# Optimization experiments

Hardware: AMD Instinct MI355X
Metric: run time of the kernel (lower is better)

Reference implementation:

```python
import jax, jax.numpy as jnp
import numpy as np

B, S, D, H = 2, 2048, 768, 12
HD = D // H  # head_dim = 64


def setup_inputs() -> dict:
    key = jax.random.key(0)
    ks = jax.random.split(key, 9)
    s = 1.0 / np.sqrt(D)
    return {
        "x": jax.random.normal(ks[0], (B, S, D), dtype=jnp.float32),
        "Wq": jax.random.normal(ks[1], (D, D), dtype=jnp.float32) * s,
        "bq": jnp.zeros((D,), dtype=jnp.float32),
        "Wk": jax.random.normal(ks[2], (D, D), dtype=jnp.float32) * s,
        "bk": jnp.zeros((D,), dtype=jnp.float32),
        "Wv": jax.random.normal(ks[3], (D, D), dtype=jnp.float32) * s,
        "bv": jnp.zeros((D,), dtype=jnp.float32),
        "Wo": jax.random.normal(ks[4], (D, D), dtype=jnp.float32) * s,
        "bo": jnpp if False else jnp.zeros((D,), dtype=jnp.float32),
    }


def reference(x, Wq, bq, Wk, bk, Wv, bv, Wo, bo):
    b, s, d = x.shape
    # projections, split heads: [b, h, s, hd]
    def proj(W, bias):
        y = x @ W + bias
        return y.reshape(b, s, H, HD).transpose(0, 2, 1, 3)

    q = proj(Wq, bq)
    k = proj(Wk, bk)
    v = proj(Wv, bv)

    scale = 1.0 / jnp.sqrt(jnp.float32(HD))
    scores = jnp.einsum("bhqd,bhkd->bhqk", q, k) * scale
    causal = jnp.tril(jnp.ones((s, s), dtype=bool))  # True where allowed
    scores = jnp.where(causal, scores, -jnp.inf)
    attn = jax.nn.softmax(scores, axis=-1)
    ctx = jnp.einsum("bhqk,bhkd->bhqd", attn, v)
    ctx = ctx.transpose(0, 2, 1, 3).reshape(b, s, d)
    return ctx @ Wo + bo
```

## Files before the change

kernel.cpp:

```cpp
#include <hip/hip_runtime.h>
#include <stdint.h>

typedef unsigned short u16;
typedef __attribute__((ext_vector_type(8))) short s16x8;
typedef __attribute__((ext_vector_type(4))) float f32x4;
typedef __attribute__((ext_vector_type(16))) float f32x16;

#define MFMA_BF16(a, b, c) __builtin_amdgcn_mfma_f32_16x16x32_bf16((a), (b), (c), 0, 0, 0)
#define MFMA32(a, b, c) __builtin_amdgcn_mfma_f32_32x32x16_bf16((a), (b), (c), 0, 0, 0)

typedef const __attribute__((address_space(1))) uint32_t* gas1_t;
typedef __attribute__((address_space(3))) uint32_t* las3_t;
#define GLDS16(dst, src) __builtin_amdgcn_global_load_lds((gas1_t)(src), (las3_t)(dst), 16, 0, 0)

static __device__ __forceinline__ u16 f2bf(float f) {
    uint32_t u = __float_as_uint(f);
    u = (u + 0x7fffu + ((u >> 16) & 1u)) >> 16;
    return (u16)u;
}
static __device__ __forceinline__ uint32_t pk2bf(float a, float b) {
    return (uint32_t)f2bf(a) | ((uint32_t)f2bf(b) << 16);
}

__global__ void k_cvt_bf16(const float* __restrict__ in, u16* __restrict__ out) {
    int i = (blockIdx.x * 256 + threadIdx.x) * 8;
    f32x4 a = *(const f32x4*)(in + i);
    f32x4 b = *(const f32x4*)(in + i + 4);
    s16x8 r;
    r[0] = (short)f2bf(a[0]); r[1] = (short)f2bf(a[1]);
    r[2] = (short)f2bf(a[2]); r[3] = (short)f2bf(a[3]);
    r[4] = (short)f2bf(b[0]); r[5] = (short)f2bf(b[1]);
    r[6] = (short)f2bf(b[2]); r[7] = (short)f2bf(b[3]);
    *(s16x8*)(out + i) = r;
}

__global__ void k_transpose_w(const float* __restrict__ w0, const float* __restrict__ w1,
                              const float* __restrict__ w2, const float* __restrict__ w3,
                              u16* __restrict__ t0, u16* __restrict__ t1,
                              u16* __restrict__ t2, u16* __restrict__ t3) {
    __shared__ float tile[32][33];
    const float* W; u16* T;
    switch (blockIdx.z) {
        case 0:  W = w0; T = t0; break;
        case 1:  W = w1; T = t1; break;
        case 2:  W = w2; T = t2; break;
        default: W = w3; T = t3; break;
    }
    int n0 = blockIdx.x * 32, k0 = blockIdx.y * 32;
    int tx = threadIdx.x, ty = threadIdx.y;
#pragma unroll
    for (int i = 0; i < 4; ++i)
        tile[ty + 8 * i][tx] = W[(size_t)(k0 + ty + 8 * i) * 768 + n0 + tx];
    __syncthreads();
#pragma unroll
    for (int i = 0; i < 4; ++i)
        T[(size_t)(n0 + ty + 8 * i) * 768 + k0 + tx] = f2bf(tile[tx][ty + 8 * i]);
}

__global__ __launch_bounds__(256) void k_gemm_qkv(
        const u16* __restrict__ A,
        const u16* __restrict__ btq, const u16* __restrict__ btk, const u16* __restrict__ btv,
        const float* __restrict__ bq, const float* __restrict__ bk, const float* __restrict__ bv,
        u16* __restrict__ outq, u16* __restrict__ outk, u16* __restrict__ outv) {
    __shared__ u16 lA[128 * 64];
    __shared__ u16 lB[64 * 64];
    const int bx = blockIdx.x, sel = bx / 12, nb = bx - sel * 12;
    const u16* Bt; const float* bias;
    if (sel == 0)      { Bt = btq; bias = bq; }
    else if (sel == 1) { Bt = btk; bias = bk; }
    else               { Bt = btv; bias = bv; }
    const int t = threadIdx.x, lane = t & 63, w = t >> 6;
    const int wr = w >> 1, wc = w & 1;
    const int c = lane & 15, g = lane >> 4;
    const int m0 = blockIdx.y * 128, n0 = nb * 64;
    f32x4 acc[4][2] = {};
    const int lr = lane >> 3, lg = lane & 7;
    const int swz8 = 8 * (lg ^ lr);
    const u16* gA = A  + (size_t)(m0 + w * 8 + lr) * 768 + swz8;
    const u16* gB = Bt + (size_t)(n0 + w * 8 + lr) * 768 + swz8;
    for (int kb = 0; kb < 768; kb += 64) {
#pragma unroll
        for (int j = 0; j < 4; ++j)
            GLDS16(&lA[j * 2048 + w * 512], gA + (size_t)j * 32 * 768 + kb);
#pragma unroll
        for (int j = 0; j < 2; ++j)
            GLDS16(&lB[j * 2048 + w * 512], gB + (size_t)j * 32 * 768 + kb);
        __syncthreads();
#pragma unroll
        for (int kh = 0; kh < 2; ++kh) {
            s16x8 af[4], bfr[2];
            const int gg = kh * 4 + g;
#pragma unroll
            for (int i = 0; i < 4; ++i) {
                const int ra = wr * 64 + i * 16 + c;
                af[i] = *(const s16x8*)&lA[ra * 64 + 8 * (gg ^ (ra & 7))];
            }
#pragma unroll
            for (int j = 0; j < 2; ++j) {
                const int rb = wc * 32 + j * 16 + c;
                bfr[j] = *(const s16x8*)&lB[rb * 64 + 8 * (gg ^ (rb & 7))];
            }
#pragma unroll
            for (int i = 0; i < 4; ++i)
#pragma unroll
                for (int j = 0; j < 2; ++j)
                    acc[i][j] = MFMA_BF16(af[i], bfr[j], acc[i][j]);
        }
        __syncthreads();
    }
    const float C2 = 0.18033688011112042f;
    const int h = nb;
    if (sel < 2) {
        u16* outp = (sel == 0) ? outq : outk;
        const float osc = (sel == 0) ? C2 : 1.0f;
#pragma unroll
        for (int i = 0; i < 4; ++i)
#pragma unroll
            for (int j = 0; j < 2; ++j) {
                const int hd = wc * 32 + j * 16 + c;
                const float bvv = bias[n0 + hd];
#pragma unroll
                for (int rr = 0; rr < 4; ++rr) {
                    const int m = m0 + wr * 64 + i * 16 + g * 4 + rr;
                    const int b = m >> 11, s = m & 2047;
                    outp[(((size_t)(b * 12 + h) * 2048 + s) << 6) + hd] =
                        f2bf((acc[i][j][rr] + bvv) * osc);
                }
            }
    } else {
#pragma unroll
        for (int i = 0; i < 4; ++i)
#pragma unroll
            for (int j = 0; j < 2; ++j) {
                const int hd = wc * 32 + j * 16 + c;
                const float bvv = bias[n0 + hd];
                const int m = m0 + wr * 64 + i * 16 + g * 4;
                const int b = m >> 11, s = m & 2047;
                uint64_t pk = (uint64_t)pk2bf(acc[i][j][0] + bvv, acc[i][j][1] + bvv) |
                              ((uint64_t)pk2bf(acc[i][j][2] + bvv, acc[i][j][3] + bvv) << 32);
                *(uint64_t*)&outv[((size_t)(b * 12 + h) * 64 + hd) * 2048 + s] = pk;
            }
    }
}

__global__ __launch_bounds__(256) void k_gemm_out(const u16* __restrict__ A,
                                                  const u16* __restrict__ Bt,
                                                  const float* __restrict__ bias,
                                                  float* __restrict__ out) {
    __shared__ u16 lA[64 * 64];
    __shared__ u16 lB[64 * 64];
    const int t = threadIdx.x;
    const int lane = t & 63, w = t >> 6;
    const int wr = w >> 1, wc = w & 1;
    const int c = lane & 15, g = lane >> 4;
    const int m0 = blockIdx.y * 64, n0 = blockIdx.x * 64;
    f32x4 acc[2][2] = {};
    const int lr = lane >> 3, lq = lane & 7;
    const int sq = (lq ^ lr) * 8;
    const u16* gA0 = A  + (size_t)(m0 + w * 16 + lr) * 768 + sq;
    const u16* gA1 = gA0 + 8 * 768;
    const u16* gB0 = Bt + (size_t)(n0 + w * 16 + lr) * 768 + sq;
    const u16* gB1 = gB0 + 8 * 768;
    u16* dA0 = &lA[w * 1024];
    u16* dA1 = &lA[w * 1024 + 512];
    u16* dB0 = &lB[w * 1024];
    u16* dB1 = &lB[w * 1024 + 512];
    for (int kb = 0; kb < 768; kb += 64) {
        GLDS16(dA0, gA0 + kb); GLDS16(dA1, gA1 + kb);
        GLDS16(dB0, gB0 + kb); GLDS16(dB1, gB1 + kb);
        __syncthreads();
#pragma unroll
        for (int st = 0; st < 2; ++st) {
            s16x8 af[2], bf[2];
            const int col = st * 32 + g * 8;
#pragma unroll
            for (int i = 0; i < 2; ++i) {
                int ra = wr * 32 + i * 16 + c;
                af[i] = *(const s16x8*)&lA[ra * 64 + (col ^ ((ra & 7) << 3))];
                int rb = wc * 32 + i * 16 + c;
                bf[i] = *(const s16x8*)&lB[rb * 64 + (col ^ ((rb & 7) << 3))];
            }
#pragma unroll
            for (int i = 0; i < 2; ++i)
#pragma unroll
                for (int j = 0; j < 2; ++j)
                    acc[i][j] = MFMA_BF16(af[i], bf[j], acc[i][j]);
        }
        __syncthreads();
    }
#pragma unroll
    for (int i = 0; i < 2; ++i)
#pragma unroll
        for (int j = 0; j < 2; ++j) {
            const int n = n0 + wc * 32 + j * 16 + c;
            const float bvv = bias[n];
#pragma unroll
            for (int rr = 0; rr < 4; ++rr) {
                const int m = m0 + wr * 32 + i * 16 + g * 4 + rr;
                out[(size_t)m * 768 + n] = acc[i][j][rr] + bvv;
            }
        }
}

__global__ __launch_bounds__(128) void k_attn(const u16* __restrict__ qw,
                                              const u16* __restrict__ kw,
                                              const u16* __restrict__ vt,
                                              u16* __restrict__ ctxb) {
    __shared__ u16 lK[2][64 * 64];
    __shared__ u16 lV[2][64 * 64];
    const int bid = blockIdx.x;
    const int qt = 31 - bid / 24;
    const int bh = bid % 24;
    const int t = threadIdx.x, lane = t & 63, w = t >> 6;
    const int l31 = lane & 31, hi = lane >> 5;
    const int q0w = qt * 64 + w * 32;
    const u16* qp = qw + (size_t)bh * 2048 * 64;
    const u16* kp = kw + (size_t)bh * 2048 * 64;
    const u16* vp = vt + (size_t)bh * 64 * 2048;
    s16x8 qf[4];
#pragma unroll
    for (int dk = 0; dk < 4; ++dk)
        qf[dk] = *(const s16x8*)&qp[(size_t)(q0w + l31) * 64 + dk * 16 + hi * 8];
    asm volatile("s_waitcnt vmcnt(0)" ::: "memory");
    const int lr = lane >> 3, lg = lane & 7;
    const int swz8 = 8 * (lg ^ lr);
    const u16* kpb = kp + (size_t)(w * 8 + lr) * 64 + swz8;
    const u16* vpb = vp + (size_t)(w * 8 + lr) * 2048 + swz8;
    const int NC = qt + 1;
    const int lastq = q0w + 31;
    f32x16 ct[2] = {};
    float m2 = -1e30f, ssum = 0.0f;
#define STAGE(bf, ch)                                                          \
    {                                                                          \
        const u16* ks_ = kpb + (size_t)(ch) * 4096;                            \
        GLDS16(&lK[bf][(w * 8) * 64], ks_);                                    \
        GLDS16(&lK[bf][(16 + w * 8) * 64], ks_ + 16 * 64);                     \
        GLDS16(&lK[bf][(32 + w * 8) * 64], ks_ + 32 * 64);                     \
        GLDS16(&lK[bf][(48 + w * 8) * 64], ks_ + 48 * 64);                     \
        const u16* vs_ = vpb + (size_t)(ch) * 64;                              \
        GLDS16(&lV[bf][(w * 8) * 64], vs_);                                    \
        GLDS16(&lV[bf][(16 + w * 8) * 64], vs_ + 16 * 2048);                   \
        GLDS16(&lV[bf][(32 + w * 8) * 64], vs_ + 32 * 2048);                   \
        GLDS16(&lV[bf][(48 + w * 8) * 64], vs_ + 48 * 2048);                   \
    }
    STAGE(0, 0);
    for (int ch = 0; ch < NC; ++ch) {
        const int bf = ch & 1, Kc = ch * 64;
        if (ch + 1 < NC) {
            STAGE(bf ^ 1, ch + 1);
            asm volatile("s_waitcnt vmcnt(8)" ::: "memory");
        } else {
            asm volatile("s_waitcnt vmcnt(0)" ::: "memory");
        }
        __builtin_amdgcn_sched_barrier(0);
        __builtin_amdgcn_s_barrier();
        {
            f32x16 st[2] = {};
            __builtin_amdgcn_s_setprio(1);
#pragma unroll
            for (int dk = 0; dk < 4; ++dk) {
                const int gr = dk * 2 + hi;
                const int r0 = l31, r1 = 32 + l31;
                s16x8 kf0 = *(const s16x8*)&lK[bf][r0 * 64 + 8 * (gr ^ (r0 & 7))];
                s16x8 kf1 = *(const s16x8*)&lK[bf][r1 * 64 + 8 * (gr ^ (r1 & 7))];
                st[0] = MFMA32(kf0, qf[dk], st[0]);
                st[1] = MFMA32(kf1, qf[dk], st[1]);
            }
            __builtin_amdgcn_s_setprio(0);
            const int qg = q0w + l31;
            float tv[32];
            if (Kc + 63 <= q0w) {
#pragma unroll
                for (int j = 0; j < 16; ++j) { tv[j] = st[0][j]; tv[16 + j] = st[1][j]; }
            } else {
                const int kb = Kc + 4 * hi;
#pragma unroll
                for (int j = 0; j < 16; ++j) {
                    const int kloc = (j & 3) + 8 * (j >> 2);
                    tv[j]      = (kb + kloc      <= qg) ? st[0][j] : -1e30f;
                    tv[16 + j] = (kb + kloc + 32 <= qg) ? st[1][j] : -1e30f;
                }
            }
            float mt = tv[0];
#pragma unroll
            for (int j = 1; j < 32; ++j) mt = fmaxf(mt, tv[j]);
            if (!__all(mt <= m2 + 8.0f)) {
                float mq = fmaxf(mt, __shfl_xor(mt, 32));
                const float mnew = fmaxf(m2, mq);
                const float fac = __builtin_amdgcn_exp2f(m2 - mnew);
                ssum *= fac;
#pragma unroll
                for (int j = 0; j < 16; ++j) { ct[0][j] *= fac; ct[1][j] *= fac; }
                m2 = mnew;
            }
            float p[32];
#pragma unroll
            for (int j = 0; j < 32; ++j) { p[j] = __builtin_amdgcn_exp2f(tv[j] - m2); ssum += p[j]; }
#pragma unroll
            for (int kt = 0; kt < 2; ++kt) {
                uint32_t pcv[8];
#pragma unroll
                for (int x = 0; x < 8; ++x) {
                    const int j = kt * 16 + 4 * (x >> 1) + 2 * (x & 1);
                    asm volatile("v_cvt_pk_bf16_f32 %0, %1, %2"
                                 : "=v"(pcv[x]) : "v"(p[j]), "v"(p[j + 1]));
                }
#pragma unroll
                for (int kl = 0; kl < 2; ++kl) {
                    const uint32_t s0 = hi ? pcv[4 * kl]     : pcv[4 * kl + 2];
                    const uint32_t s1 = hi ? pcv[4 * kl + 1] : pcv[4 * kl + 3];
                    const uint32_t r0 = __shfl_xor(s0, 32);
                    const uint32_t r1 = __shfl_xor(s1, 32);
                    union { uint32_t u[4]; s16x8 v; } pf;
                    pf.u[0] = hi ? r0 : pcv[4 * kl];
                    pf.u[1] = hi ? r1 : pcv[4 * kl + 1];
                    pf.u[2] = hi ? pcv[4 * kl + 2] : r0;
                    pf.u[3] = hi ? pcv[4 * kl + 3] : r1;
                    const int gr = (kt * 2 + kl) * 2 + hi;
                    const int rv0 = l31, rv1 = 32 + l31;
                    s16x8 vf0 = *(const s16x8*)&lV[bf][rv0 * 64 + 8 * (gr ^ (rv0 & 7))];
                    s16x8 vf1 = *(const s16x8*)&lV[bf][rv1 * 64 + 8 * (gr ^ (rv1 & 7))];
                    __builtin_amdgcn_s_setprio(1);
                    ct[0] = MFMA32(vf0, pf.v, ct[0]);
                    ct[1] = MFMA32(vf1, pf.v, ct[1]);
                    __builtin_amdgcn_s_setprio(0);
                }
            }
        }
        __builtin_amdgcn_s_barrier();
    }
    ssum += __shfl_xor(ssum, 32);
    const float inv = 1.0f / ssum;
    const int b = bh / 12, h = bh - b * 12;
    const size_t base = (size_t)(b * 2048 + q0w + l31) * 768 + h * 64;
#pragma unroll
    for (int ht = 0; ht < 2; ++ht)
#pragma unroll
        for (int a = 0; a < 4; ++a) {
            const int hd = ht * 32 + 8 * a + 4 * hi;
            uint64_t pk = (uint64_t)pk2bf(ct[ht][4 * a] * inv, ct[ht][4 * a + 1] * inv) |
                          ((uint64_t)pk2bf(ct[ht][4 * a + 2] * inv, ct[ht][4 * a + 3] * inv) << 32);
            *(uint64_t*)&ctxb[base + hd] = pk;
        }
#undef STAGE
}

extern "C" void kernel_launch(void* const* d_in, const int* in_sizes, int n_in,
                              void* d_out, int out_size, void* d_ws, size_t ws_size,
                              hipStream_t stream) {
    (void)in_sizes; (void)n_in; (void)out_size; (void)ws_size;
    const float* x  = (const float*)d_in[0];
    const float* Wq = (const float*)d_in[1];
    const float* bq = (const float*)d_in[2];
    const float* Wk = (const float*)d_in[3];
    const float* bk = (const float*)d_in[4];
    const float* Wv = (const float*)d_in[5];
    const float* bv = (const float*)d_in[6];
    const float* Wo = (const float*)d_in[7];
    const float* bo = (const float*)d_in[8];
    char* ws = (char*)d_ws;
    u16* xb   = (u16*)(ws);
    u16* wqt  = (u16*)(ws + 6291456);
    u16* wkt  = (u16*)(ws + 7471104);
    u16* wvt  = (u16*)(ws + 8650752);
    u16* wot  = (u16*)(ws + 9830400);
    u16* qwv  = (u16*)(ws + 11010048);
    u16* kwv  = (u16*)(ws + 17301504);
    u16* vtw  = (u16*)(ws + 23592960);
    u16* ctx  = (u16*)(ws + 29884416);
    float* out = (float*)d_out;

    k_cvt_bf16<<<1536, 256, 0, stream>>>(x, xb);
    k_transpose_w<<<dim3(24, 24, 4), dim3(32, 8), 0, stream>>>(Wq, Wk, Wv, Wo, wqt, wkt, wvt, wot);
    k_gemm_qkv<<<dim3(36, 32), 256, 0, stream>>>(xb, wqt, wkt, wvt, bq, bk, bv, qwv, kwv, vtw);
    k_attn<<<768, 128, 0, stream>>>(qwv, kwv, vtw, ctx);
    k_gemm_out<<<dim3(12, 64), 256, 0, stream>>>(ctx, wot, bo, out);
}
```

Before: 172.6 us.

## Split causal attention KV range into segments with a separate combine kernel

```diff
diff --git a/kernel.cpp b/kernel.cpp
--- a/kernel.cpp
+++ b/kernel.cpp
@@ -20,6 +20,9 @@
 }
 static __device__ __forceinline__ uint32_t pk2bf(float a, float b) {
     return (uint32_t)f2bf(a) | ((uint32_t)f2bf(b) << 16);
+}
+static __device__ __forceinline__ float bf2f(u16 h) {
+    return __uint_as_float(((uint32_t)h) << 16);
 }
 
 __global__ void k_cvt_bf16(const float* __restrict__ in, u16* __restrict__ out) {
@@ -205,15 +208,26 @@
 __global__ __launch_bounds__(128) void k_attn(const u16* __restrict__ qw,
                                               const u16* __restrict__ kw,
                                               const u16* __restrict__ vt,
-                                              u16* __restrict__ ctxb) {
+                                              u16* __restrict__ ctxb,
+                                              u16* __restrict__ pctx,
+                                              float* __restrict__ pm,
+                                              float* __restrict__ ps) {
     __shared__ u16 lK[2][64 * 64];
     __shared__ u16 lV[2][64 * 64];
     const int bid = blockIdx.x;
-    const int qt = 31 - bid / 24;
-    const int bh = bid % 24;
+    const int slot = bid / 24, bh = bid - slot * 24;
+    int qt64, seg;
+    if (slot < 32)      { qt64 = 31 - (slot >> 2); seg = slot & 3; }
+    else if (slot < 56) { const int u = slot - 32; const int d3 = u / 3; qt64 = 23 - d3; seg = u - d3 * 3; }
+    else if (slot < 72) { const int u = slot - 56; qt64 = 15 - (u >> 1); seg = u & 1; }
+    else                { qt64 = 79 - slot; seg = 0; }
+    const int nseg = (qt64 >> 3) + 1;
+    const int ch0 = seg * 8;
+    const int nchunks = qt64 + 1 - ch0;
+    const int nch = nchunks < 8 ? nchunks : 8;
     const int t = threadIdx.x, lane = t & 63, w = t >> 6;
     const int l31 = lane & 31, hi = lane >> 5;
-    const int q0w = qt * 64 + w * 32;
+    const int q0w = qt64 * 64 + w * 32;
     const u16* qp = qw + (size_t)bh * 2048 * 64;
     const u16* kp = kw + (size_t)bh * 2048 * 64;
     const u16* vp = vt + (size_t)bh * 64 * 2048;
@@ -226,7 +240,6 @@
     const int swz8 = 8 * (lg ^ lr);
     const u16* kpb = kp + (size_t)(w * 8 + lr) * 64 + swz8;
     const u16* vpb = vp + (size_t)(w * 8 + lr) * 2048 + swz8;
-    const int NC = qt + 1;
     const int lastq = q0w + 31;
     f32x16 ct[2] = {};
     float m2 = -1e30f, ssum = 0.0f;
@@ -243,18 +256,18 @@
         GLDS16(&lV[bf][(32 + w * 8) * 64], vs_ + 32 * 2048);                   \
         GLDS16(&lV[bf][(48 + w * 8) * 64], vs_ + 48 * 2048);                   \
     }
-    STAGE(0, 0);
-    for (int ch = 0; ch < NC; ++ch) {
-        const int bf = ch & 1, Kc = ch * 64;
-        if (ch + 1 < NC) {
-            STAGE(bf ^ 1, ch + 1);
+    STAGE(0, ch0);
+    for (int ci = 0; ci < nch; ++ci) {
+        const int bf = ci & 1, Kc = (ch0 + ci) * 64;
+        if (ci + 1 < nch) {
+            STAGE(bf ^ 1, ch0 + ci + 1);
             asm volatile("s_waitcnt vmcnt(8)" ::: "memory");
         } else {
             asm volatile("s_waitcnt vmcnt(0)" ::: "memory");
         }
         __builtin_amdgcn_sched_barrier(0);
         __builtin_amdgcn_s_barrier();
-        {
+        if (Kc <= lastq) {
             f32x16 st[2] = {};
             __builtin_amdgcn_s_setprio(1);
 #pragma unroll
@@ -281,9 +294,14 @@
                     tv[16 + j] = (kb + kloc + 32 <= qg) ? st[1][j] : -1e30f;
                 }
             }
-            float mt = tv[0];
-#pragma unroll
-            for (int j = 1; j < 32; ++j) mt = fmaxf(mt, tv[j]);
+            float x16[16], x8[8], x4[4];
+#pragma unroll
+            for (int j = 0; j < 16; ++j) x16[j] = fmaxf(tv[j], tv[j + 16]);
+#pragma unroll
+            for (int j = 0; j < 8; ++j) x8[j] = fmaxf(x16[j], x16[j + 8]);
+#pragma unroll
+            for (int j = 0; j < 4; ++j) x4[j] = fmaxf(x8[j], x8[j + 4]);
+            const float mt = fmaxf(fmaxf(x4[0], x4[1]), fmaxf(x4[2], x4[3]));
             if (!__all(mt <= m2 + 8.0f)) {
                 float mq = fmaxf(mt, __shfl_xor(mt, 32));
                 const float mnew = fmaxf(m2, mq);
@@ -295,7 +313,15 @@
             }
             float p[32];
 #pragma unroll
-            for (int j = 0; j < 32; ++j) { p[j] = __builtin_amdgcn_exp2f(tv[j] - m2); ssum += p[j]; }
+            for (int j = 0; j < 32; ++j) p[j] = __builtin_amdgcn_exp2f(tv[j] - m2);
+            float y16[16], y8[8], y4[4];
+#pragma unroll
+            for (int j = 0; j < 16; ++j) y16[j] = p[j] + p[j + 16];
+#pragma unroll
+            for (int j = 0; j < 8; ++j) y8[j] = y16[j] + y16[j + 8];
+#pragma unroll
+            for (int j = 0; j < 4; ++j) y4[j] = y8[j] + y8[j + 4];
+            ssum += (y4[0] + y4[1]) + (y4[2] + y4[3]);
 #pragma unroll
             for (int kt = 0; kt < 2; ++kt) {
                 uint32_t pcv[8];
@@ -307,15 +333,12 @@
                 }
 #pragma unroll
                 for (int kl = 0; kl < 2; ++kl) {
-                    const uint32_t s0 = hi ? pcv[4 * kl]     : pcv[4 * kl + 2];
-                    const uint32_t s1 = hi ? pcv[4 * kl + 1] : pcv[4 * kl + 3];
-                    const uint32_t r0 = __shfl_xor(s0, 32);
-                    const uint32_t r1 = __shfl_xor(s1, 32);
+                    uint32_t a0 = pcv[4 * kl],     b0 = pcv[4 * kl + 2];
+                    uint32_t a1 = pcv[4 * kl + 1], b1 = pcv[4 * kl + 3];
+                    asm volatile("v_permlane32_swap_b32 %0, %1" : "+v"(a0), "+v"(b0));
+                    asm volatile("v_permlane32_swap_b32 %0, %1" : "+v"(a1), "+v"(b1));
                     union { uint32_t u[4]; s16x8 v; } pf;
-                    pf.u[0] = hi ? r0 : pcv[4 * kl];
-                    pf.u[1] = hi ? r1 : pcv[4 * kl + 1];
-                    pf.u[2] = hi ? pcv[4 * kl + 2] : r0;
-                    pf.u[3] = hi ? pcv[4 * kl + 3] : r1;
+                    pf.u[0] = a0; pf.u[1] = a1; pf.u[2] = b0; pf.u[3] = b1;
                     const int gr = (kt * 2 + kl) * 2 + hi;
                     const int rv0 = l31, rv1 = 32 + l31;
                     s16x8 vf0 = *(const s16x8*)&lV[bf][rv0 * 64 + 8 * (gr ^ (rv0 & 7))];
@@ -329,20 +352,89 @@
         }
         __builtin_amdgcn_s_barrier();
     }
-    ssum += __shfl_xor(ssum, 32);
-    const float inv = 1.0f / ssum;
+    if (nseg == 1) {
+        ssum += __shfl_xor(ssum, 32);
+        const float inv = 1.0f / ssum;
+        const int b = bh / 12, h = bh - b * 12;
+        const size_t base = (size_t)(b * 2048 + q0w + l31) * 768 + h * 64;
+#pragma unroll
+        for (int ht = 0; ht < 2; ++ht)
+#pragma unroll
+            for (int a = 0; a < 4; ++a) {
+                const int hd = ht * 32 + 8 * a + 4 * hi;
+                uint64_t pk = (uint64_t)pk2bf(ct[ht][4 * a] * inv, ct[ht][4 * a + 1] * inv) |
+                              ((uint64_t)pk2bf(ct[ht][4 * a + 2] * inv, ct[ht][4 * a + 3] * inv) << 32);
+                *(uint64_t*)&ctxb[base + hd] = pk;
+            }
+    } else {
+        const float srow = ssum + __shfl_xor(ssum, 32);
+        const int ti = (bh * 32 + qt64) * 4 + seg;
+        const int row = w * 32 + l31;
+        u16* pp = &pctx[(size_t)ti * 4096 + row * 64];
+#pragma unroll
+        for (int ht = 0; ht < 2; ++ht)
+#pragma unroll
+            for (int a = 0; a < 4; ++a) {
+                const int hd = ht * 32 + 8 * a + 4 * hi;
+                uint64_t pk = (uint64_t)pk2bf(ct[ht][4 * a], ct[ht][4 * a + 1]) |
+                              ((uint64_t)pk2bf(ct[ht][4 * a + 2], ct[ht][4 * a + 3]) << 32);
+                *(uint64_t*)&pp[hd] = pk;
+            }
+        if (hi == 0) {
+            pm[ti * 64 + row] = m2;
+            ps[ti * 64 + row] = srow;
+        }
+    }
+#undef STAGE
+}
+
+__global__ __launch_bounds__(256) void k_attn_combine(const u16* __restrict__ pctx,
+                                                      const float* __restrict__ pm,
+                                                      const float* __restrict__ ps,
+                                                      u16* __restrict__ ctxb) {
+    const int bh = blockIdx.x, qt64 = blockIdx.y + 8;
+    const int nseg = (qt64 >> 3) + 1;
+    const int t = threadIdx.x, row = t >> 2, h0 = (t & 3) * 16;
+    const int tb = (bh * 32 + qt64) * 4;
+    float mv[4], sv[4];
+#pragma unroll
+    for (int s = 0; s < 4; ++s) {
+        mv[s] = (s < nseg) ? pm[(tb + s) * 64 + row] : -1e30f;
+        sv[s] = (s < nseg) ? ps[(tb + s) * 64 + row] : 0.0f;
+    }
+    const float mstar = fmaxf(fmaxf(mv[0], mv[1]), fmaxf(mv[2], mv[3]));
+    float wv[4], S = 0.0f;
+#pragma unroll
+    for (int s = 0; s < 4; ++s) {
+        wv[s] = __builtin_amdgcn_exp2f(mv[s] - mstar);
+        S += wv[s] * sv[s];
+    }
+    float acc[16] = {};
+#pragma unroll
+    for (int s = 0; s < 4; ++s) {
+        if (s < nseg) {
+            const u16* pp = &pctx[(size_t)(tb + s) * 4096 + row * 64 + h0];
+            const float wgt = wv[s];
+#pragma unroll
+            for (int e = 0; e < 2; ++e) {
+                s16x8 v = *(const s16x8*)(pp + e * 8);
+#pragma unroll
+                for (int x = 0; x < 8; ++x)
+                    acc[e * 8 + x] += wgt * bf2f((u16)v[x]);
+            }
+        }
+    }
+    const float inv = 1.0f / S;
     const int b = bh / 12, h = bh - b * 12;
-    const size_t base = (size_t)(b * 2048 + q0w + l31) * 768 + h * 64;
-#pragma unroll
-    for (int ht = 0; ht < 2; ++ht)
-#pragma unroll
-        for (int a = 0; a < 4; ++a) {
-            const int hd = ht * 32 + 8 * a + 4 * hi;
-            uint64_t pk = (uint64_t)pk2bf(ct[ht][4 * a] * inv, ct[ht][4 * a + 1] * inv) |
-                          ((uint64_t)pk2bf(ct[ht][4 * a + 2] * inv, ct[ht][4 * a + 3] * inv) << 32);
-            *(uint64_t*)&ctxb[base + hd] = pk;
-        }
-#undef STAGE
+    u16* op = &ctxb[(size_t)(b * 2048 + qt64 * 64 + row) * 768 + h * 64 + h0];
+    s16x8 o0, o1;
+#pragma unroll
+    for (int x = 0; x < 8; ++x) {
+        o0[x] = (short)f2bf(acc[x] * inv);
+        o1[x] = (short)f2bf(acc[8 + x] * inv);
+    }
+    *(s16x8*)op = o0;
+    *(s16x8*)(op + 8) = o1;
 }
 
 extern "C" void kernel_launch(void* const* d_in, const int* in_sizes, int n_in,
@@ -368,11 +460,15 @@
     u16* kwv  = (u16*)(ws + 17301504);
     u16* vtw  = (u16*)(ws + 23592960);
     u16* ctx  = (u16*)(ws + 29884416);
+    u16* pctx = (u16*)(ws + 36175872);
+    float* pm = (float*)(ws + 61341696);
+    float* psu= (float*)(ws + 62128128);
     float* out = (float*)d_out;
 
     k_cvt_bf16<<<1536, 256, 0, stream>>>(x, xb);
     k_transpose_w<<<dim3(24, 24, 4), dim3(32, 8), 0, stream>>>(Wq, Wk, Wv, Wo, wqt, wkt, wvt, wot);
     k_gemm_qkv<<<dim3(36, 32), 256, 0, stream>>>(xb, wqt, wkt, wvt, bq, bk, bv, qwv, kwv, vtw);
-    k_attn<<<768, 128, 0, stream>>>(qwv, kwv, vtw, ctx);
+    k_attn<<<1920, 128, 0, stream>>>(qwv, kwv, vtw, ctx, pctx, pm, psu);
+    k_attn_combine<<<dim3(24, 24), 256, 0, stream>>>(pctx, pm, psu, ctx);
     k_gemm_out<<<dim3(12, 64), 256, 0, stream>>>(ctx, wot, bo, out);
 }
```

After: 162.1 us. 1.06x faster.
